# Optimization experiments

Measured on AMD Instinct MI355X. Metric: run time of the kernel, lower is better.

The kernel has to match this reference:

```python
import jax, jax.numpy as jnp
import numpy as np

B, SECL, WORDL = 16, 8, 512
S = SECL * WORDL
H, E, V, NOOV = 256, 128, 50000, 32
EOS = 3
FSIZE = 2  # config.mode == 'train'


def setup_inputs() -> dict:
    key = jax.random.key(0)
    ks = jax.random.split(key, 24)
    g = lambda i, shape, s=0.02: jax.random.normal(ks[i], shape, jnp.float32) * s
    inp = jax.random.randint(ks[0], (B,), 0, V)
    inp = inp.at[:4].set(EOS)  # exercise focus-update branch
    h = g(1, (B, H), 0.1)
    c = g(2, (B, H), 0.1)
    enc_outputs = g(3, (B, S, 2 * H), 1.0)
    enc_feature = g(4, (B, S, 2 * H), 0.1)
    enc_sec_output = g(5, (B, SECL, 2 * H), 1.0)
    enc_mask = jnp.ones((B, S), jnp.float32)
    sec_mask = jnp.ones((B, SECL), jnp.float32)
    prev_context = g(6, (B, 2 * H), 0.1)
    zeros_oov = jnp.zeros((B, NOOV), jnp.float32)
    enc_input_oov = jax.random.randint(ks[7], (B, S), 0, V + NOOV)
    coverage = jnp.zeros((B, S), jnp.float32)
    # sparse nonneg focus distribution over sections (guaranteed >=1 nonzero/row)
    u = jax.random.uniform(ks[8], (B, SECL))
    f = u * (u > 0.5)
    fb = jax.nn.one_hot(jnp.argmax(u, axis=1), SECL)
    f = jnp.where(f.sum(1, keepdims=True) > 0, f, fb)
    focus = f / f.sum(1, keepdims=True)
    params = dict(
        embedding=g(9, (V, E)),
        W_comb=g(10, (E, 2 * H + E)), b_comb=jnp.zeros((E,), jnp.float32),
        W_ih=g(11, (4 * H, E)), W_hh=g(12, (4 * H, H)),
        b_ih=jnp.zeros((4 * H,), jnp.float32), b_hh=jnp.zeros((4 * H,), jnp.float32),
        W_d=g(13, (2 * H, 2 * H)), b_d=jnp.zeros((2 * H,), jnp.float32),
        W_feat=g(14, (2 * H, 2 * H)), v_sec=g(15, (2 * H,)),
        W_dec=g(16, (2 * H, 2 * H)), b_dec=jnp.zeros((2 * H,), jnp.float32),
        w_cov=g(17, (2 * H,)), v_att=g(18, (2 * H,)),
        W_pgen=g(19, (1, 4 * H + E)), b_pgen=jnp.zeros((1,), jnp.float32),
        W_out=g(20, (V, 3 * H)), b_out=g(21, (V,)),
    )
    return dict(inp=inp, h=h, c=c, enc_outputs=enc_outputs, enc_feature=enc_feature,
                enc_sec_output=enc_sec_output, enc_mask=enc_mask, sec_mask=sec_mask,
                prev_context=prev_context, zeros_oov=zeros_oov, enc_input_oov=enc_input_oov,
                coverage=coverage, focus=focus, **params)


def _focus_update(focus, sad):
    # rem_mask: positions from the first nonzero of focus onward
    fz = jnp.cumprod((focus == 0).astype(sad.dtype), axis=1)
    rem_mask = (fz == 0).astype(sad.dtype)
    focus_index = jnp.sum(fz, axis=1).astype(jnp.int32)  # index of first nonzero
    focus_mask = jax.nn.one_hot(focus_index, SECL, dtype=sad.dtype)
    rem_ex = rem_mask - focus_mask
    focus_beta = sad * focus_mask
    rem_beta = sad * rem_ex
    max_rem_beta = rem_beta.max(axis=1)
    max_rem_ind = jnp.argmax(rem_beta, axis=1)
    compare = (focus_beta.max(axis=1) * 2 > max_rem_beta).astype(sad.dtype)[:, None]
    # train branch
    src = (max_rem_beta != 0).astype(sad.dtype)[:, None]
    max_rem_mask = jax.nn.one_hot(max_rem_ind, SECL, dtype=sad.dtype) * src
    cp2 = jnp.cumprod((max_rem_mask == 0).astype(sad.dtype), axis=1)
    after = (cp2 == 0).astype(sad.dtype) - max_rem_mask
    amb = sad * after
    mam_mask = (jax.nn.one_hot(jnp.argmax(amb, axis=1), SECL, dtype=sad.dtype)
                * (amb.max(axis=1) != 0).astype(sad.dtype)[:, None])
    case_f = focus_beta + sad * max_rem_mask
    case_r = sad * (max_rem_mask + mam_mask)
    fu = compare * case_f + (1 - compare) * case_r
    return fu / fu.sum(1, keepdims=True)


def reference(inp, h, c, enc_outputs, enc_feature, enc_sec_output, enc_mask, sec_mask,
              prev_context, zeros_oov, enc_input_oov, coverage, focus,
              embedding, W_comb, b_comb, W_ih, W_hh, b_ih, b_hh,
              W_d, b_d, W_feat, v_sec, W_dec, b_dec, w_cov, v_att,
              W_pgen, b_pgen, W_out, b_out):
    inp_is_eos = (inp == EOS).astype(jnp.float32)[:, None]  # [B,1] -> bcast over secL
    emb = embedding[inp]  # [B,E]
    x = jnp.concatenate([prev_context, emb], axis=1) @ W_comb.T + b_comb  # [B,E]
    # single LSTM step (torch gate order i,f,g,o)
    gates = x @ W_ih.T + b_ih + h @ W_hh.T + b_hh
    gi_, gf_, gg_, go_ = jnp.split(gates, 4, axis=1)
    c_new = jax.nn.sigmoid(gf_) * c + jax.nn.sigmoid(gi_) * jnp.tanh(gg_)
    h_new = jax.nn.sigmoid(go_) * jnp.tanh(c_new)
    dec_state = jnp.concatenate([h_new, c_new], axis=1)  # [B,2H]
    # section attention
    feat = enc_sec_output @ W_feat.T  # [B,secL,2H]
    d = dec_state @ W_d.T + b_d
    sc = jnp.tanh(feat + d[:, None, :]) @ v_sec  # [B,secL]
    sad = jax.nn.softmax(sc, axis=1) * sec_mask
    sad = sad / sad.sum(1, keepdims=True)
    # hard-attention focus update (only where input was EOS)
    fu = _focus_update(focus, sad)
    focus = inp_is_eos * fu + (1 - inp_is_eos) * focus
    # word attention with coverage
    dfeat = dec_state @ W_dec.T + b_dec
    att = enc_feature + dfeat[:, None, :] + coverage[:, :, None] * w_cov[None, None, :]
    score = jnp.tanh(att) @ v_att  # [B,S]
    score3 = score.reshape(B, SECL, WORDL)
    topk_focus, gidx = jax.lax.top_k(focus, FSIZE)  # [B,FSIZE]
    bidx = jnp.arange(B)[:, None]
    score_g = score3[bidx, gidx].reshape(B, FSIZE * WORDL)
    mask_g = enc_mask.reshape(B, SECL, WORDL)[bidx, gidx].reshape(B, FSIZE * WORDL)
    af = jax.nn.softmax(score_g, axis=1) * mask_g
    af = af / af.sum(1, keepdims=True)
    af = topk_focus[:, :, None] * af.reshape(B, FSIZE, WORDL)
    attn = jnp.zeros((B, SECL, WORDL), af.dtype).at[bidx, gidx].set(af).reshape(B, S)
    attn = attn / attn.sum(1, keepdims=True)
    context = jnp.einsum('bs,bsd->bd', attn, enc_outputs)  # [B,2H]
    coverage = coverage + attn
    # pointer-generator
    p_gen = jax.nn.sigmoid(jnp.concatenate([context, dec_state, x], axis=1) @ W_pgen.T + b_pgen)
    logits = jnp.concatenate([h_new, context], axis=1) @ W_out.T + b_out
    vocab_dist = jax.nn.softmax(logits, axis=1)
    vext = jnp.concatenate([p_gen * vocab_dist, zeros_oov], axis=1)  # [B,V+NOOV]
    final = vext.at[bidx, enc_input_oov].add((1 - p_gen) * attn)
    return final, h_new, c_new, context, attn, coverage, focus, sad
```

## Files before the change

### kernel.cpp

```cpp
#include <hip/hip_runtime.h>
#include <math.h>

#define NB 16
#define SECL 8
#define WORDL 512
#define SS 4096
#define HH 256
#define EE 128
#define VV 50000
#define NOOV 32
#define VO 50032
#define EOS_ID 3
#define H2 512
#define KOUT 768
#define NCH 13
#define CHSZ 4096

#define OFF_FINAL 0
#define OFF_H    800512
#define OFF_C    804608
#define OFF_CTX  808704
#define OFF_ATTN 816896
#define OFF_COV  882432
#define OFF_FOC  947968
#define OFF_SAD  948096

#define WX     0
#define WD     2048
#define WDF    10240
#define WSC    18432
#define WGI    18560
#define WTF    18592
#define WSG    18624
#define WPART  35008
#define WPG    166080
#define WPM    166096
#define WPS    166304
#define WLG    166512

__device__ __forceinline__ float sigm(float x){ return 1.f/(1.f+__expf(-x)); }
__device__ __forceinline__ float tfast(float x){
  float ax = fabsf(x);
  float e  = __expf(-2.f*ax);
  float t  = (1.f-e)/(1.f+e);
  return x < 0.f ? -t : t;
}
__device__ __forceinline__ float dot4(float acc, float4 a, float4 b){
  acc = fmaf(a.x,b.x,acc); acc = fmaf(a.y,b.y,acc);
  acc = fmaf(a.z,b.z,acc); acc = fmaf(a.w,b.w,acc);
  return acc;
}
__device__ __forceinline__ float dot2(float acc, float2 a, float2 b){
  acc = fmaf(a.x,b.x,acc); acc = fmaf(a.y,b.y,acc);
  return acc;
}
__device__ __forceinline__ float mergep(float a, float b, int k, int lane){
  float send = (lane & k) ? a : b;
  float recv = __shfl_xor(send, k);
  return (lane & k) ? b + recv : a + recv;
}
__device__ __forceinline__ float reduce8(float acc[8], int lane){
  float m0 = mergep(acc[0], acc[1], 1, lane);
  float m1 = mergep(acc[2], acc[3], 1, lane);
  float m2 = mergep(acc[4], acc[5], 1, lane);
  float m3 = mergep(acc[6], acc[7], 1, lane);
  float n0 = mergep(m0, m1, 2, lane);
  float n1 = mergep(m2, m3, 2, lane);
  float p  = mergep(n0, n1, 4, lane);
  p += __shfl_xor(p, 8);
  p += __shfl_xor(p, 16);
  p += __shfl_xor(p, 32);
  return p;
}

__global__ void __launch_bounds__(256)
k_x(const int* __restrict__ inp, const float* __restrict__ pc,
    const float* __restrict__ emb, const float* __restrict__ Wc,
    const float* __restrict__ bc, float* __restrict__ ws){
  int lane = threadIdx.x & 63;
  int gw = blockIdx.x*4 + (threadIdx.x >> 6);
  int bg = gw & 1, e = gw >> 1;
  float4 z = {0,0,0,0};
  float4 i0[8], i1[8], i2[8];
  #pragma unroll
  for(int j=0;j<8;j++){
    int b = bg*8 + j;
    i0[j] = *(const float4*)(pc + b*H2 + lane*4);
    i1[j] = *(const float4*)(pc + b*H2 + 256 + lane*4);
    i2[j] = (lane < 32) ? *(const float4*)(emb + (size_t)inp[b]*EE + lane*4) : z;
  }
  const float* wr = Wc + (size_t)e*(H2+EE);
  float4 w0 = *(const float4*)(wr + lane*4);
  float4 w1 = *(const float4*)(wr + 256 + lane*4);
  float4 w2 = (lane < 32) ? *(const float4*)(wr + 512 + lane*4) : z;
  float acc[8];
  #pragma unroll
  for(int j=0;j<8;j++){
    float a = dot4(0.f, w0, i0[j]);
    a = dot4(a, w1, i1[j]);
    a = dot4(a, w2, i2[j]);
    acc[j] = a;
  }
  float p = reduce8(acc, lane);
  if(lane < 8) ws[WX + (bg*8+lane)*EE + e] = p + bc[e];
}

__global__ void __launch_bounds__(256)
k_gates(const float* __restrict__ h, const float* __restrict__ c,
        const float* __restrict__ Wih, const float* __restrict__ Whh,
        const float* __restrict__ bih, const float* __restrict__ bhh,
        const float* __restrict__ ws, float* __restrict__ out){
  __shared__ float g_lds[4][8];
  int lane = threadIdx.x & 63;
  int wv   = threadIdx.x >> 6;
  int j  = blockIdx.x >> 1;
  int bg = blockIdx.x & 1;
  float2 xb[8]; float4 hb[8];
  #pragma unroll
  for(int q=0;q<8;q++){
    int b = bg*8 + q;
    xb[q] = *(const float2*)(ws + WX + b*EE + lane*2);
    hb[q] = *(const float4*)(h + b*HH + lane*4);
  }
  int r = wv*HH + j;
  float2 wx = *(const float2*)(Wih + (size_t)r*EE + lane*2);
  float4 wh = *(const float4*)(Whh + (size_t)r*HH + lane*4);
  float acc[8];
  #pragma unroll
  for(int q=0;q<8;q++)
    acc[q] = dot4(dot2(0.f, wx, xb[q]), wh, hb[q]);
  float p = reduce8(acc, lane);
  if(lane < 8) g_lds[wv][lane] = p + bih[r] + bhh[r];
  __syncthreads();
  if(threadIdx.x < 8){
    int b = bg*8 + threadIdx.x;
    float g0 = g_lds[0][threadIdx.x], g1 = g_lds[1][threadIdx.x];
    float g2 = g_lds[2][threadIdx.x], g3 = g_lds[3][threadIdx.x];
    float cn = sigm(g1)*c[b*HH + j] + sigm(g0)*tfast(g2);
    float hn = sigm(g3)*tfast(cn);
    out[OFF_H + b*HH + j] = hn;
    out[OFF_C + b*HH + j] = cn;
  }
}

__global__ void __launch_bounds__(256)
k_dd(const float* __restrict__ Wd, const float* __restrict__ bd,
     const float* __restrict__ Wdec, const float* __restrict__ bdec,
     const float* __restrict__ out, float* __restrict__ ws){
  int lane = threadIdx.x & 63;
  int gw = blockIdx.x*4 + (threadIdx.x >> 6);
  int bg = gw & 1, sel = (gw >> 1) & 1, j = gw >> 2;
  float4 d0[8], d1[8];
  #pragma unroll
  for(int q=0;q<8;q++){
    int b = bg*8 + q;
    d0[q] = *(const float4*)(out + OFF_H + b*HH + lane*4);
    d1[q] = *(const float4*)(out + OFF_C + b*HH + lane*4);
  }
  const float* wr = (sel ? Wdec : Wd) + (size_t)j*H2;
  float4 w0 = *(const float4*)(wr + lane*4);
  float4 w1 = *(const float4*)(wr + 256 + lane*4);
  float acc[8];
  #pragma unroll
  for(int q=0;q<8;q++)
    acc[q] = dot4(dot4(0.f, w0, d0[q]), w1, d1[q]);
  float p = reduce8(acc, lane);
  if(lane < 8) ws[(sel ? WDF : WD) + (bg*8+lane)*H2 + j] = p + (sel ? bdec : bd)[j];
}

__global__ void __launch_bounds__(256)
k_sec(const float* __restrict__ eso, const float* __restrict__ Wf,
      const float* __restrict__ vsec, float* __restrict__ ws){
  __shared__ float red[4];
  int lane = threadIdx.x & 63;
  int wv   = threadIdx.x >> 6;
  int bl = blockIdx.x; int b = bl >> 3;
  const float* ep = eso + (size_t)bl*H2;
  float4 es0 = *(const float4*)(ep + lane*4);
  float4 es1 = *(const float4*)(ep + 256 + lane*4);
  const float* dp = ws + WD + b*H2;
  float local = 0.f;
  for(int t=0;t<16;t++){
    int j0 = wv*8 + t*32;
    float acc[8];
    #pragma unroll
    for(int jj=0;jj<8;jj++){
      const float* wr = Wf + (size_t)(j0+jj)*H2;
      float4 w0 = *(const float4*)(wr + lane*4);
      float4 w1 = *(const float4*)(wr + 256 + lane*4);
      acc[jj] = dot4(dot4(0.f, w0, es0), w1, es1);
    }
    float p = reduce8(acc, lane);
    if(lane < 8){
      int j = j0 + lane;
      local += tfast(p + dp[j]) * vsec[j];
    }
  }
  local += __shfl_xor(local, 1);
  local += __shfl_xor(local, 2);
  local += __shfl_xor(local, 4);
  if(lane == 0) red[wv] = local;
  __syncthreads();
  if(threadIdx.x == 0) ws[WSC + bl] = red[0]+red[1]+red[2]+red[3];
}

__global__ void k_focus(const int* __restrict__ inp, const float* __restrict__ smask,
                        const float* __restrict__ focus_in, float* __restrict__ ws,
                        float* __restrict__ out){
  int b = threadIdx.x;
  if(b >= NB) return;
  float sc[SECL], sad[SECL], f[SECL];
  float mx = -1e30f;
  for(int l=0;l<SECL;l++){ sc[l] = ws[WSC + b*SECL + l]; mx = fmaxf(mx, sc[l]); }
  float sum = 0.f;
  for(int l=0;l<SECL;l++){ sad[l] = __expf(sc[l]-mx); sum += sad[l]; }
  float s2 = 0.f;
  for(int l=0;l<SECL;l++){ sad[l] = sad[l]/sum * smask[b*SECL+l]; s2 += sad[l]; }
  for(int l=0;l<SECL;l++){ sad[l] /= s2; out[OFF_SAD + b*SECL + l] = sad[l]; }
  for(int l=0;l<SECL;l++) f[l] = focus_in[b*SECL+l];
  int fi = SECL;
  for(int l=0;l<SECL;l++){ if(f[l] != 0.f){ fi = l; break; } }
  float rem[SECL];
  for(int l=0;l<SECL;l++) rem[l] = (l > fi) ? sad[l] : 0.f;
  float mrb = rem[0]; int mri = 0;
  for(int l=1;l<SECL;l++){ if(rem[l] > mrb){ mrb = rem[l]; mri = l; } }
  float fbm = (fi < SECL) ? sad[fi] : 0.f;
  int cmp = (fbm*2.f > mrb);
  int src = (mrb != 0.f);
  float amb[SECL];
  for(int l=0;l<SECL;l++) amb[l] = (src && l > mri) ? sad[l] : 0.f;
  float am = amb[0]; int ai = 0;
  for(int l=1;l<SECL;l++){ if(amb[l] > am){ am = amb[l]; ai = l; } }
  float fu[SECL]; float fs = 0.f;
  for(int l=0;l<SECL;l++){
    float mrm = (src && l == mri) ? 1.f : 0.f;
    float mam = ((am != 0.f) && l == ai) ? 1.f : 0.f;
    float cf = ((l==fi) ? sad[l] : 0.f) + sad[l]*mrm;
    float cr = sad[l]*(mrm + mam);
    fu[l] = cmp ? cf : cr;
    fs += fu[l];
  }
  float eos = (inp[b] == EOS_ID) ? 1.f : 0.f;
  float fo[SECL];
  for(int l=0;l<SECL;l++){
    fo[l] = eos*(fu[l]/fs) + (1.f-eos)*f[l];
    out[OFF_FOC + b*SECL + l] = fo[l];
  }
  float v1 = fo[0]; int i1 = 0;
  for(int l=1;l<SECL;l++){ if(fo[l] > v1){ v1 = fo[l]; i1 = l; } }
  float v2 = -1e30f; int i2 = 0;
  for(int l=0;l<SECL;l++){ if(l != i1 && fo[l] > v2){ v2 = fo[l]; i2 = l; } }
  ((int*)ws)[WGI + b*2]     = i1;
  ((int*)ws)[WGI + b*2 + 1] = i2;
  ws[WTF + b*2]     = v1;
  ws[WTF + b*2 + 1] = v2;
}

__global__ void k_score(const float* __restrict__ ef, const float* __restrict__ cov,
                        const float* __restrict__ wcov, const float* __restrict__ vatt,
                        float* __restrict__ ws){
  int lane = threadIdx.x & 63;
  int o = blockIdx.x*4 + (threadIdx.x >> 6);
  int b = o >> 10, fidx = (o >> 9) & 1, w = o & 511;
  int g = ((const int*)ws)[WGI + b*2 + fidx];
  int s = g*WORDL + w;
  const float* e  = ef + ((size_t)(b*SS + s))*H2;
  const float* df = ws + WDF + b*H2;
  float cv = cov[b*SS + s];
  int j = lane*4;
  float local = 0.f;
  #pragma unroll
  for(int half=0; half<2; half++){
    int jj = j + half*256;
    float4 a  = *(const float4*)(e+jj);
    float4 d4 = *(const float4*)(df+jj);
    float4 wc = *(const float4*)(wcov+jj);
    float4 va = *(const float4*)(vatt+jj);
    local += tfast(a.x + d4.x + cv*wc.x)*va.x;
    local += tfast(a.y + d4.y + cv*wc.y)*va.y;
    local += tfast(a.z + d4.z + cv*wc.z)*va.z;
    local += tfast(a.w + d4.w + cv*wc.w)*va.w;
  }
  for(int off=32; off>0; off>>=1) local += __shfl_xor(local, off);
  if(lane == 0) ws[WSG + o] = local;
}

__global__ void k_af(const float* __restrict__ emask, const float* __restrict__ cov,
                     float* __restrict__ ws, float* __restrict__ out){
  __shared__ float es[1024];
  __shared__ float red[256];
  int b = blockIdx.x, tid = threadIdx.x;
  int g0 = ((int*)ws)[WGI+b*2], g1 = ((int*)ws)[WGI+b*2+1];
  float tf0 = ws[WTF+b*2], tf1 = ws[WTF+b*2+1];
  float lm = -1e30f;
  for(int i=tid;i<1024;i+=256) lm = fmaxf(lm, ws[WSG + b*1024 + i]);
  red[tid] = lm; __syncthreads();
  for(int off=128; off; off>>=1){
    if(tid < off) red[tid] = fmaxf(red[tid], red[tid+off]);
    __syncthreads();
  }
  float mx = red[0]; __syncthreads();
  float ls0 = 0.f, ls1 = 0.f;
  for(int i=tid;i<1024;i+=256){
    int fidx = i >> 9, w = i & 511;
    int g = fidx ? g1 : g0;
    float m = emask[b*SS + g*WORDL + w];
    float ev = __expf(ws[WSG + b*1024 + i] - mx)*m;
    es[i] = ev;
    if(fidx) ls1 += ev; else ls0 += ev;
  }
  red[tid] = ls0; __syncthreads();
  for(int off=128; off; off>>=1){ if(tid<off) red[tid]+=red[tid+off]; __syncthreads(); }
  float sum0 = red[0]; __syncthreads();
  red[tid] = ls1; __syncthreads();
  for(int off=128; off; off>>=1){ if(tid<off) red[tid]+=red[tid+off]; __syncthreads(); }
  float sum1 = red[0]; __syncthreads();
  float inv = 1.f/(tf0*sum0 + tf1*sum1);
  for(int s=tid;s<SS;s+=256){
    int sec = s >> 9, w = s & 511;
    float a = 0.f;
    if(sec == g0)      a = tf0*es[w]*inv;
    else if(sec == g1) a = tf1*es[512+w]*inv;
    out[OFF_ATTN + b*SS + s] = a;
    out[OFF_COV  + b*SS + s] = cov[b*SS+s] + a;
  }
}

__global__ void k_ctxp(const float* __restrict__ eo, const float* __restrict__ out,
                       float* __restrict__ ws){
  int blk = blockIdx.x; int b = blk >> 4, ch = blk & 15;
  int d = threadIdx.x;
  int g0 = ((const int*)ws)[WGI + b*2];
  int g1 = ((const int*)ws)[WGI + b*2 + 1];
  float a0 = 0.f, a1 = 0.f;
  #pragma unroll 4
  for(int p = ch*64; p < ch*64 + 64; p++){
    int s = ((p >> 9) ? g1 : g0)*WORDL + (p & 511);
    float a = out[OFF_ATTN + b*SS + s];
    const float* ep = eo + ((size_t)(b*SS + s))*H2;
    a0 = fmaf(a, ep[d],       a0);
    a1 = fmaf(a, ep[d+256],   a1);
  }
  ws[WPART + (size_t)blk*H2 + d]       = a0;
  ws[WPART + (size_t)blk*H2 + d + 256] = a1;
}

__global__ void k_ctx(const float* __restrict__ Wp, const float* __restrict__ bp,
                      float* __restrict__ ws, float* __restrict__ out){
  __shared__ float red[256];
  int b = blockIdx.x, tid = threadIdx.x;
  float c0 = 0.f, c1 = 0.f;
  for(int ch=0; ch<16; ch++){
    c0 += ws[WPART + (size_t)(b*16+ch)*H2 + tid];
    c1 += ws[WPART + (size_t)(b*16+ch)*H2 + tid + 256];
  }
  out[OFF_CTX + b*H2 + tid]       = c0;
  out[OFF_CTX + b*H2 + tid + 256] = c1;
  float hn = out[OFF_H + b*HH + tid];
  float cn = out[OFF_C + b*HH + tid];
  float pv = c0*Wp[tid] + c1*Wp[tid+256] + hn*Wp[512+tid] + cn*Wp[768+tid];
  if(tid < EE) pv = fmaf(ws[WX + b*EE + tid], Wp[1024+tid], pv);
  red[tid] = pv; __syncthreads();
  for(int off=128; off; off>>=1){ if(tid<off) red[tid]+=red[tid+off]; __syncthreads(); }
  if(tid == 0) ws[WPG + b] = sigm(red[0] + bp[0]);
}

__global__ void __launch_bounds__(256,3)
k_logits(const float* __restrict__ Wout, const float* __restrict__ bout,
         const float* __restrict__ out, float* __restrict__ ws){
  int lane = threadIdx.x & 63;
  int wv   = threadIdx.x >> 6;
  int bg   = wv & 1;
  int rh   = wv >> 1;
  float4 hb0[8], hb1[8], hb2[8];
  #pragma unroll
  for(int j=0;j<8;j++){
    int b = bg*8 + j;
    hb0[j] = *(const float4*)(out + OFF_H   + b*HH + lane*4);
    hb1[j] = *(const float4*)(out + OFF_CTX + b*H2 + lane*4);
    hb2[j] = *(const float4*)(out + OFF_CTX + b*H2 + 256 + lane*4);
  }
  int v = blockIdx.x*32 + rh;
  int vc = v < VV ? v : VV-1;
  const float* wp = Wout + (size_t)vc*KOUT + lane*4;
  float4 a0 = *(const float4*)(wp);
  float4 a1 = *(const float4*)(wp+256);
  float4 a2 = *(const float4*)(wp+512);
  #pragma unroll 2
  for(int r=0;r<16;r++){
    int vn = v + 2;
    int vnc = vn < VV ? vn : VV-1;
    const float* np = Wout + (size_t)vnc*KOUT + lane*4;
    float4 n0 = *(const float4*)(np);
    float4 n1 = *(const float4*)(np+256);
    float4 n2 = *(const float4*)(np+512);
    float acc[8];
    #pragma unroll
    for(int j=0;j<8;j++){
      float a = dot4(0.f, a0, hb0[j]);
      a = dot4(a, a1, hb1[j]);
      a = dot4(a, a2, hb2[j]);
      acc[j] = a;
    }
    float p = reduce8(acc, lane);
    if(v < VV && lane < 8)
      ws[WLG + (size_t)(bg*8+lane)*VV + v] = p + bout[v];
    a0 = n0; a1 = n1; a2 = n2;
    v = vn;
  }
}

__global__ void k_vms(float* __restrict__ ws){
  __shared__ float rm[256], rs[256];
  int blk = blockIdx.x; int b = blk/NCH, ch = blk%NCH;
  int tid = threadIdx.x;
  int v0 = ch*CHSZ; int v1 = v0+CHSZ; if(v1 > VV) v1 = VV;
  float mt = -1e30f, st = 0.f;
  for(int v=v0+tid; v<v1; v+=256){
    float x = ws[WLG + (size_t)b*VV + v];
    if(x > mt){ st = st*__expf(mt - x) + 1.f; mt = x; }
    else       st += __expf(x - mt);
  }
  rm[tid] = mt; rs[tid] = st; __syncthreads();
  for(int off=128; off; off>>=1){
    if(tid < off){
      float ma = rm[tid], mb = rm[tid+off];
      float M = fmaxf(ma, mb);
      rs[tid] = rs[tid]*__expf(ma-M) + rs[tid+off]*__expf(mb-M);
      rm[tid] = M;
    }
    __syncthreads();
  }
  if(tid == 0){ ws[WPM + blk] = rm[0]; ws[WPS + blk] = rs[0]; }
}

__global__ void k_final(const float* __restrict__ zoov, float* __restrict__ ws,
                        float* __restrict__ out){
  int blk = blockIdx.x; int b = blk/NCH, ch = blk%NCH;
  float mx = -1e30f, sm = 0.f;
  for(int i=0;i<NCH;i++){ mx = fmaxf(mx, ws[WPM + b*NCH + i]); }
  for(int i=0;i<NCH;i++){ sm += ws[WPS + b*NCH + i]*__expf(ws[WPM + b*NCH + i] - mx); }
  float scale = ws[WPG + b] / sm;
  int v0 = ch*CHSZ; int v1 = v0+CHSZ; if(v1 > VO) v1 = VO;
  for(int v=v0+threadIdx.x; v<v1; v+=256){
    float r;
    if(v < VV) r = scale*__expf(ws[WLG + (size_t)b*VV + v] - mx);
    else       r = zoov[b*NOOV + v - VV];
    out[OFF_FINAL + (size_t)b*VO + v] = r;
  }
}

__global__ void k_scatter(const int* __restrict__ oov, const float* __restrict__ ws,
                          float* __restrict__ out){
  int blk = blockIdx.x; int b = blk >> 4;
  int s = (blk & 15)*256 + threadIdx.x;
  float a = out[OFF_ATTN + b*SS + s];
  if(a != 0.f){
    float w = (1.f - ws[WPG + b])*a;
    atomicAdd(out + OFF_FINAL + (size_t)b*VO + oov[b*SS + s], w);
  }
}

extern "C" void kernel_launch(void* const* d_in, const int* in_sizes, int n_in,
                              void* d_out, int out_size, void* d_ws, size_t ws_size,
                              hipStream_t stream){
  const int*   inp   = (const int*)  d_in[0];
  const float* h     = (const float*)d_in[1];
  const float* c     = (const float*)d_in[2];
  const float* eo    = (const float*)d_in[3];
  const float* efeat = (const float*)d_in[4];
  const float* eso   = (const float*)d_in[5];
  const float* emask = (const float*)d_in[6];
  const float* smask = (const float*)d_in[7];
  const float* pctx  = (const float*)d_in[8];
  const float* zoov  = (const float*)d_in[9];
  const int*   oov   = (const int*)  d_in[10];
  const float* cov   = (const float*)d_in[11];
  const float* foc   = (const float*)d_in[12];
  const float* emb   = (const float*)d_in[13];
  const float* Wc    = (const float*)d_in[14];
  const float* bc    = (const float*)d_in[15];
  const float* Wih   = (const float*)d_in[16];
  const float* Whh   = (const float*)d_in[17];
  const float* bih   = (const float*)d_in[18];
  const float* bhh   = (const float*)d_in[19];
  const float* Wd    = (const float*)d_in[20];
  const float* bd    = (const float*)d_in[21];
  const float* Wf    = (const float*)d_in[22];
  const float* vsec  = (const float*)d_in[23];
  const float* Wdec  = (const float*)d_in[24];
  const float* bdec  = (const float*)d_in[25];
  const float* wcov  = (const float*)d_in[26];
  const float* vatt  = (const float*)d_in[27];
  const float* Wp    = (const float*)d_in[28];
  const float* bp    = (const float*)d_in[29];
  const float* Wout  = (const float*)d_in[30];
  const float* bout  = (const float*)d_in[31];
  float* out = (float*)d_out;
  float* ws  = (float*)d_ws;

  k_x      <<<64,   256, 0, stream>>>(inp, pctx, emb, Wc, bc, ws);
  k_gates  <<<512,  256, 0, stream>>>(h, c, Wih, Whh, bih, bhh, ws, out);
  k_dd     <<<512,  256, 0, stream>>>(Wd, bd, Wdec, bdec, out, ws);
  k_sec    <<<128,  256, 0, stream>>>(eso, Wf, vsec, ws);
  k_focus  <<<1,     64, 0, stream>>>(inp, smask, foc, ws, out);
  k_score  <<<4096, 256, 0, stream>>>(efeat, cov, wcov, vatt, ws);
  k_af     <<<16,   256, 0, stream>>>(emask, cov, ws, out);
  k_ctxp   <<<256,  256, 0, stream>>>(eo, out, ws);
  k_ctx    <<<16,   256, 0, stream>>>(Wp, bp, ws, out);
  k_logits <<<1563, 256, 0, stream>>>(Wout, bout, out, ws);
  k_vms    <<<208,  256, 0, stream>>>(ws);
  k_final  <<<208,  256, 0, stream>>>(zoov, ws, out);
  k_scatter<<<256,  256, 0, stream>>>(oov, ws, out);
}
```

Measured before the change: 139.5 us.

## Fuse front-end kernels into cooperative grid-synced kernel and restructure logits pipelining

Replaces the five small front-end kernels (x projection, LSTM gates, decoder projections, section scores, focus update) with one cooperative kernel that uses grid.sync between phases, removing launch gaps. The section-score phase is split four ways per section so all 512 blocks take part, with partial sums combined in the focus step. If the cooperative launch fails, the code falls back to the old separate launches. Separately, the logits kernel now has each wave handle 8 consecutive vocab rows with a two-deep register prefetch, and the grid doubles to 3125 blocks with no tail bounds check.

```diff
diff --git a/kernel.cpp b/kernel.cpp
--- a/kernel.cpp
+++ b/kernel.cpp
@@ -1,5 +1,8 @@
 #include <hip/hip_runtime.h>
+#include <hip/hip_cooperative_groups.h>
 #include <math.h>
+
+namespace cg = cooperative_groups;
 
 #define NB 16
 #define SECL 8
@@ -37,6 +40,7 @@
 #define WPM    166096
 #define WPS    166304
 #define WLG    166512
+#define WSCP   966512
 
 __device__ __forceinline__ float sigm(float x){ return 1.f/(1.f+__expf(-x)); }
 __device__ __forceinline__ float tfast(float x){
@@ -73,12 +77,10 @@
   return p;
 }
 
-__global__ void __launch_bounds__(256)
-k_x(const int* __restrict__ inp, const float* __restrict__ pc,
-    const float* __restrict__ emb, const float* __restrict__ Wc,
-    const float* __restrict__ bc, float* __restrict__ ws){
-  int lane = threadIdx.x & 63;
-  int gw = blockIdx.x*4 + (threadIdx.x >> 6);
+
+__device__ __forceinline__ void phase_x(int gw, int lane,
+    const int* inp, const float* pc, const float* emb,
+    const float* Wc, const float* bc, float* ws){
   int bg = gw & 1, e = gw >> 1;
   float4 z = {0,0,0,0};
   float4 i0[8], i1[8], i2[8];
@@ -105,69 +107,205 @@
   if(lane < 8) ws[WX + (bg*8+lane)*EE + e] = p + bc[e];
 }
 
+__device__ __forceinline__ void phase_gates(int blk, int wv, int lane, int tid,
+    const float* h, const float* c, const float* Wih, const float* Whh,
+    const float* bih, const float* bhh, const float* ws, float* out,
+    float (*g_lds)[8]){
+  int j  = blk >> 1;
+  int bg = blk & 1;
+  float2 xb[8]; float4 hb[8];
+  #pragma unroll
+  for(int q=0;q<8;q++){
+    int b = bg*8 + q;
+    xb[q] = *(const float2*)(ws + WX + b*EE + lane*2);
+    hb[q] = *(const float4*)(h + b*HH + lane*4);
+  }
+  int r = wv*HH + j;
+  float2 wx = *(const float2*)(Wih + (size_t)r*EE + lane*2);
+  float4 wh = *(const float4*)(Whh + (size_t)r*HH + lane*4);
+  float acc[8];
+  #pragma unroll
+  for(int q=0;q<8;q++)
+    acc[q] = dot4(dot2(0.f, wx, xb[q]), wh, hb[q]);
+  float p = reduce8(acc, lane);
+  if(lane < 8) g_lds[wv][lane] = p + bih[r] + bhh[r];
+  __syncthreads();
+  if(tid < 8){
+    int b = bg*8 + tid;
+    float g0 = g_lds[0][tid], g1 = g_lds[1][tid];
+    float g2 = g_lds[2][tid], g3 = g_lds[3][tid];
+    float cn = sigm(g1)*c[b*HH + j] + sigm(g0)*tfast(g2);
+    float hn = sigm(g3)*tfast(cn);
+    out[OFF_H + b*HH + j] = hn;
+    out[OFF_C + b*HH + j] = cn;
+  }
+}
+
+__device__ __forceinline__ void phase_dd(int gw, int lane,
+    const float* Wd, const float* bd, const float* Wdec, const float* bdec,
+    const float* out, float* ws){
+  int bg = gw & 1, sel = (gw >> 1) & 1, j = gw >> 2;
+  float4 d0[8], d1[8];
+  #pragma unroll
+  for(int q=0;q<8;q++){
+    int b = bg*8 + q;
+    d0[q] = *(const float4*)(out + OFF_H + b*HH + lane*4);
+    d1[q] = *(const float4*)(out + OFF_C + b*HH + lane*4);
+  }
+  const float* wr = (sel ? Wdec : Wd) + (size_t)j*H2;
+  float4 w0 = *(const float4*)(wr + lane*4);
+  float4 w1 = *(const float4*)(wr + 256 + lane*4);
+  float acc[8];
+  #pragma unroll
+  for(int q=0;q<8;q++)
+    acc[q] = dot4(dot4(0.f, w0, d0[q]), w1, d1[q]);
+  float p = reduce8(acc, lane);
+  if(lane < 8) ws[(sel ? WDF : WD) + (bg*8+lane)*H2 + j] = p + (sel ? bdec : bd)[j];
+}
+
+__device__ __forceinline__ void focus_body(int b, float sc[SECL],
+    const int* inp, const float* smask, const float* focus_in,
+    float* ws, float* out){
+  float sad[SECL], f[SECL];
+  float mx = -1e30f;
+  for(int l=0;l<SECL;l++) mx = fmaxf(mx, sc[l]);
+  float sum = 0.f;
+  for(int l=0;l<SECL;l++){ sad[l] = __expf(sc[l]-mx); sum += sad[l]; }
+  float s2 = 0.f;
+  for(int l=0;l<SECL;l++){ sad[l] = sad[l]/sum * smask[b*SECL+l]; s2 += sad[l]; }
+  for(int l=0;l<SECL;l++){ sad[l] /= s2; out[OFF_SAD + b*SECL + l] = sad[l]; }
+  for(int l=0;l<SECL;l++) f[l] = focus_in[b*SECL+l];
+  int fi = SECL;
+  for(int l=0;l<SECL;l++){ if(f[l] != 0.f){ fi = l; break; } }
+  float rem[SECL];
+  for(int l=0;l<SECL;l++) rem[l] = (l > fi) ? sad[l] : 0.f;
+  float mrb = rem[0]; int mri = 0;
+  for(int l=1;l<SECL;l++){ if(rem[l] > mrb){ mrb = rem[l]; mri = l; } }
+  float fbm = (fi < SECL) ? sad[fi] : 0.f;
+  int cmp = (fbm*2.f > mrb);
+  int src = (mrb != 0.f);
+  float amb[SECL];
+  for(int l=0;l<SECL;l++) amb[l] = (src && l > mri) ? sad[l] : 0.f;
+  float am = amb[0]; int ai = 0;
+  for(int l=1;l<SECL;l++){ if(amb[l] > am){ am = amb[l]; ai = l; } }
+  float fu[SECL]; float fs = 0.f;
+  for(int l=0;l<SECL;l++){
+    float mrm = (src && l == mri) ? 1.f : 0.f;
+    float mam = ((am != 0.f) && l == ai) ? 1.f : 0.f;
+    float cf = ((l==fi) ? sad[l] : 0.f) + sad[l]*mrm;
+    float cr = sad[l]*(mrm + mam);
+    fu[l] = cmp ? cf : cr;
+    fs += fu[l];
+  }
+  float eos = (inp[b] == EOS_ID) ? 1.f : 0.f;
+  float fo[SECL];
+  for(int l=0;l<SECL;l++){
+    fo[l] = eos*(fu[l]/fs) + (1.f-eos)*f[l];
+    out[OFF_FOC + b*SECL + l] = fo[l];
+  }
+  float v1 = fo[0]; int i1 = 0;
+  for(int l=1;l<SECL;l++){ if(fo[l] > v1){ v1 = fo[l]; i1 = l; } }
+  float v2 = -1e30f; int i2 = 0;
+  for(int l=0;l<SECL;l++){ if(l != i1 && fo[l] > v2){ v2 = fo[l]; i2 = l; } }
+  ((int*)ws)[WGI + b*2]     = i1;
+  ((int*)ws)[WGI + b*2 + 1] = i2;
+  ws[WTF + b*2]     = v1;
+  ws[WTF + b*2 + 1] = v2;
+}
+
+__global__ void __launch_bounds__(256)
+k_front2(const int* __restrict__ inp, const float* __restrict__ pc,
+         const float* __restrict__ emb, const float* __restrict__ Wc,
+         const float* __restrict__ bc,
+         const float* __restrict__ h, const float* __restrict__ c,
+         const float* __restrict__ Wih, const float* __restrict__ Whh,
+         const float* __restrict__ bih, const float* __restrict__ bhh,
+         const float* __restrict__ Wd, const float* __restrict__ bd,
+         const float* __restrict__ Wdec, const float* __restrict__ bdec,
+         const float* __restrict__ eso, const float* __restrict__ Wf,
+         const float* __restrict__ vsec,
+         const float* __restrict__ smask, const float* __restrict__ foc,
+         float* __restrict__ ws, float* __restrict__ out){
+  cg::grid_group grid = cg::this_grid();
+  __shared__ float g_lds[4][8];
+  __shared__ float red[4];
+  int tid  = threadIdx.x;
+  int lane = tid & 63;
+  int wv   = tid >> 6;
+  int blk  = blockIdx.x;
+
+  if(blk < 64) phase_x(blk*4 + wv, lane, inp, pc, emb, Wc, bc, ws);
+  grid.sync();
+  phase_gates(blk, wv, lane, tid, h, c, Wih, Whh, bih, bhh, ws, out, g_lds);
+  grid.sync();
+  phase_dd(blk*4 + wv, lane, Wd, bd, Wdec, bdec, out, ws);
+  grid.sync();
+  {
+    int bl = blk >> 2, part = blk & 3;
+    int b = bl >> 3;
+    const float* ep = eso + (size_t)bl*H2;
+    float4 es0 = *(const float4*)(ep + lane*4);
+    float4 es1 = *(const float4*)(ep + 256 + lane*4);
+    const float* dp = ws + WD + b*H2;
+    float local = 0.f;
+    for(int tt=0;tt<4;tt++){
+      int t = part*4 + tt;
+      int j0 = wv*8 + t*32;
+      float acc[8];
+      #pragma unroll
+      for(int jj=0;jj<8;jj++){
+        const float* wr = Wf + (size_t)(j0+jj)*H2;
+        float4 w0 = *(const float4*)(wr + lane*4);
+        float4 w1 = *(const float4*)(wr + 256 + lane*4);
+        acc[jj] = dot4(dot4(0.f, w0, es0), w1, es1);
+      }
+      float p = reduce8(acc, lane);
+      if(lane < 8){
+        int j = j0 + lane;
+        local += tfast(p + dp[j]) * vsec[j];
+      }
+    }
+    local += __shfl_xor(local, 1);
+    local += __shfl_xor(local, 2);
+    local += __shfl_xor(local, 4);
+    if(lane == 0) red[wv] = local;
+    __syncthreads();
+    if(tid == 0) ws[WSCP + blk] = red[0]+red[1]+red[2]+red[3];
+  }
+  grid.sync();
+  if(blk == 0 && tid < NB){
+    int b = tid;
+    float sc[SECL];
+    for(int l=0;l<SECL;l++){
+      int bl = b*SECL + l;
+      sc[l] = ws[WSCP + bl*4] + ws[WSCP + bl*4+1]
+            + ws[WSCP + bl*4+2] + ws[WSCP + bl*4+3];
+    }
+    focus_body(b, sc, inp, smask, foc, ws, out);
+  }
+}
+
+__global__ void __launch_bounds__(256)
+k_x(const int* __restrict__ inp, const float* __restrict__ pc,
+    const float* __restrict__ emb, const float* __restrict__ Wc,
+    const float* __restrict__ bc, float* __restrict__ ws){
+  phase_x(blockIdx.x*4 + (threadIdx.x>>6), threadIdx.x & 63, inp, pc, emb, Wc, bc, ws);
+}
 __global__ void __launch_bounds__(256)
 k_gates(const float* __restrict__ h, const float* __restrict__ c,
         const float* __restrict__ Wih, const float* __restrict__ Whh,
         const float* __restrict__ bih, const float* __restrict__ bhh,
         const float* __restrict__ ws, float* __restrict__ out){
   __shared__ float g_lds[4][8];
-  int lane = threadIdx.x & 63;
-  int wv   = threadIdx.x >> 6;
-  int j  = blockIdx.x >> 1;
-  int bg = blockIdx.x & 1;
-  float2 xb[8]; float4 hb[8];
-  #pragma unroll
-  for(int q=0;q<8;q++){
-    int b = bg*8 + q;
-    xb[q] = *(const float2*)(ws + WX + b*EE + lane*2);
-    hb[q] = *(const float4*)(h + b*HH + lane*4);
-  }
-  int r = wv*HH + j;
-  float2 wx = *(const float2*)(Wih + (size_t)r*EE + lane*2);
-  float4 wh = *(const float4*)(Whh + (size_t)r*HH + lane*4);
-  float acc[8];
-  #pragma unroll
-  for(int q=0;q<8;q++)
-    acc[q] = dot4(dot2(0.f, wx, xb[q]), wh, hb[q]);
-  float p = reduce8(acc, lane);
-  if(lane < 8) g_lds[wv][lane] = p + bih[r] + bhh[r];
-  __syncthreads();
-  if(threadIdx.x < 8){
-    int b = bg*8 + threadIdx.x;
-    float g0 = g_lds[0][threadIdx.x], g1 = g_lds[1][threadIdx.x];
-    float g2 = g_lds[2][threadIdx.x], g3 = g_lds[3][threadIdx.x];
-    float cn = sigm(g1)*c[b*HH + j] + sigm(g0)*tfast(g2);
-    float hn = sigm(g3)*tfast(cn);
-    out[OFF_H + b*HH + j] = hn;
-    out[OFF_C + b*HH + j] = cn;
-  }
-}
-
+  phase_gates(blockIdx.x, threadIdx.x>>6, threadIdx.x&63, threadIdx.x,
+              h, c, Wih, Whh, bih, bhh, ws, out, g_lds);
+}
 __global__ void __launch_bounds__(256)
 k_dd(const float* __restrict__ Wd, const float* __restrict__ bd,
      const float* __restrict__ Wdec, const float* __restrict__ bdec,
      const float* __restrict__ out, float* __restrict__ ws){
-  int lane = threadIdx.x & 63;
-  int gw = blockIdx.x*4 + (threadIdx.x >> 6);
-  int bg = gw & 1, sel = (gw >> 1) & 1, j = gw >> 2;
-  float4 d0[8], d1[8];
-  #pragma unroll
-  for(int q=0;q<8;q++){
-    int b = bg*8 + q;
-    d0[q] = *(const float4*)(out + OFF_H + b*HH + lane*4);
-    d1[q] = *(const float4*)(out + OFF_C + b*HH + lane*4);
-  }
-  const float* wr = (sel ? Wdec : Wd) + (size_t)j*H2;
-  float4 w0 = *(const float4*)(wr + lane*4);
-  float4 w1 = *(const float4*)(wr + 256 + lane*4);
-  float acc[8];
-  #pragma unroll
-  for(int q=0;q<8;q++)
-    acc[q] = dot4(dot4(0.f, w0, d0[q]), w1, d1[q]);
-  float p = reduce8(acc, lane);
-  if(lane < 8) ws[(sel ? WDF : WD) + (bg*8+lane)*H2 + j] = p + (sel ? bdec : bd)[j];
-}
-
+  phase_dd(blockIdx.x*4 + (threadIdx.x>>6), threadIdx.x&63, Wd, bd, Wdec, bdec, out, ws);
+}
 __global__ void __launch_bounds__(256)
 k_sec(const float* __restrict__ eso, const float* __restrict__ Wf,
       const float* __restrict__ vsec, float* __restrict__ ws){
@@ -203,58 +341,16 @@
   __syncthreads();
   if(threadIdx.x == 0) ws[WSC + bl] = red[0]+red[1]+red[2]+red[3];
 }
-
 __global__ void k_focus(const int* __restrict__ inp, const float* __restrict__ smask,
                         const float* __restrict__ focus_in, float* __restrict__ ws,
                         float* __restrict__ out){
   int b = threadIdx.x;
   if(b >= NB) return;
-  float sc[SECL], sad[SECL], f[SECL];
-  float mx = -1e30f;
-  for(int l=0;l<SECL;l++){ sc[l] = ws[WSC + b*SECL + l]; mx = fmaxf(mx, sc[l]); }
-  float sum = 0.f;
-  for(int l=0;l<SECL;l++){ sad[l] = __expf(sc[l]-mx); sum += sad[l]; }
-  float s2 = 0.f;
-  for(int l=0;l<SECL;l++){ sad[l] = sad[l]/sum * smask[b*SECL+l]; s2 += sad[l]; }
-  for(int l=0;l<SECL;l++){ sad[l] /= s2; out[OFF_SAD + b*SECL + l] = sad[l]; }
-  for(int l=0;l<SECL;l++) f[l] = focus_in[b*SECL+l];
-  int fi = SECL;
-  for(int l=0;l<SECL;l++){ if(f[l] != 0.f){ fi = l; break; } }
-  float rem[SECL];
-  for(int l=0;l<SECL;l++) rem[l] = (l > fi) ? sad[l] : 0.f;
-  float mrb = rem[0]; int mri = 0;
-  for(int l=1;l<SECL;l++){ if(rem[l] > mrb){ mrb = rem[l]; mri = l; } }
-  float fbm = (fi < SECL) ? sad[fi] : 0.f;
-  int cmp = (fbm*2.f > mrb);
-  int src = (mrb != 0.f);
-  float amb[SECL];
-  for(int l=0;l<SECL;l++) amb[l] = (src && l > mri) ? sad[l] : 0.f;
-  float am = amb[0]; int ai = 0;
-  for(int l=1;l<SECL;l++){ if(amb[l] > am){ am = amb[l]; ai = l; } }
-  float fu[SECL]; float fs = 0.f;
-  for(int l=0;l<SECL;l++){
-    float mrm = (src && l == mri) ? 1.f : 0.f;
-    float mam = ((am != 0.f) && l == ai) ? 1.f : 0.f;
-    float cf = ((l==fi) ? sad[l] : 0.f) + sad[l]*mrm;
-    float cr = sad[l]*(mrm + mam);
-    fu[l] = cmp ? cf : cr;
-    fs += fu[l];
-  }
-  float eos = (inp[b] == EOS_ID) ? 1.f : 0.f;
-  float fo[SECL];
-  for(int l=0;l<SECL;l++){
-    fo[l] = eos*(fu[l]/fs) + (1.f-eos)*f[l];
-    out[OFF_FOC + b*SECL + l] = fo[l];
-  }
-  float v1 = fo[0]; int i1 = 0;
-  for(int l=1;l<SECL;l++){ if(fo[l] > v1){ v1 = fo[l]; i1 = l; } }
-  float v2 = -1e30f; int i2 = 0;
-  for(int l=0;l<SECL;l++){ if(l != i1 && fo[l] > v2){ v2 = fo[l]; i2 = l; } }
-  ((int*)ws)[WGI + b*2]     = i1;
-  ((int*)ws)[WGI + b*2 + 1] = i2;
-  ws[WTF + b*2]     = v1;
-  ws[WTF + b*2 + 1] = v2;
-}
+  float sc[SECL];
+  for(int l=0;l<SECL;l++) sc[l] = ws[WSC + b*SECL + l];
+  focus_body(b, sc, inp, smask, focus_in, ws, out);
+}
+
 
 __global__ void k_score(const float* __restrict__ ef, const float* __restrict__ cov,
                         const float* __restrict__ wcov, const float* __restrict__ vatt,
@@ -380,33 +476,37 @@
     hb1[j] = *(const float4*)(out + OFF_CTX + b*H2 + lane*4);
     hb2[j] = *(const float4*)(out + OFF_CTX + b*H2 + 256 + lane*4);
   }
-  int v = blockIdx.x*32 + rh;
-  int vc = v < VV ? v : VV-1;
-  const float* wp = Wout + (size_t)vc*KOUT + lane*4;
-  float4 a0 = *(const float4*)(wp);
-  float4 a1 = *(const float4*)(wp+256);
-  float4 a2 = *(const float4*)(wp+512);
-  #pragma unroll 2
-  for(int r=0;r<16;r++){
-    int vn = v + 2;
-    int vnc = vn < VV ? vn : VV-1;
-    const float* np = Wout + (size_t)vnc*KOUT + lane*4;
-    float4 n0 = *(const float4*)(np);
-    float4 n1 = *(const float4*)(np+256);
-    float4 n2 = *(const float4*)(np+512);
+  int v0 = blockIdx.x*16 + rh*8;
+  const float* w0p = Wout + (size_t)v0*KOUT + lane*4;
+  float4 A0 = *(const float4*)(w0p);
+  float4 A1 = *(const float4*)(w0p+256);
+  float4 A2 = *(const float4*)(w0p+512);
+  const float* w1p = w0p + KOUT;
+  float4 B0 = *(const float4*)(w1p);
+  float4 B1 = *(const float4*)(w1p+256);
+  float4 B2 = *(const float4*)(w1p+512);
+  #pragma unroll
+  for(int r=0;r<8;r++){
+    float4 C0=A0, C1=A1, C2=A2;
+    if(r < 6){
+      const float* np = w0p + (size_t)(r+2)*KOUT;
+      C0 = *(const float4*)(np);
+      C1 = *(const float4*)(np+256);
+      C2 = *(const float4*)(np+512);
+    }
     float acc[8];
     #pragma unroll
     for(int j=0;j<8;j++){
-      float a = dot4(0.f, a0, hb0[j]);
-      a = dot4(a, a1, hb1[j]);
-      a = dot4(a, a2, hb2[j]);
+      float a = dot4(0.f, A0, hb0[j]);
+      a = dot4(a, A1, hb1[j]);
+      a = dot4(a, A2, hb2[j]);
       acc[j] = a;
     }
     float p = reduce8(acc, lane);
-    if(v < VV && lane < 8)
-      ws[WLG + (size_t)(bg*8+lane)*VV + v] = p + bout[v];
-    a0 = n0; a1 = n1; a2 = n2;
-    v = vn;
+    int v = v0 + r;
+    if(lane < 8) ws[WLG + (size_t)(bg*8+lane)*VV + v] = p + bout[v];
+    A0=B0; A1=B1; A2=B2;
+    B0=C0; B1=C1; B2=C2;
   }
 }
 
@@ -499,16 +599,27 @@
   float* out = (float*)d_out;
   float* ws  = (float*)d_ws;
 
-  k_x      <<<64,   256, 0, stream>>>(inp, pctx, emb, Wc, bc, ws);
-  k_gates  <<<512,  256, 0, stream>>>(h, c, Wih, Whh, bih, bhh, ws, out);
-  k_dd     <<<512,  256, 0, stream>>>(Wd, bd, Wdec, bdec, out, ws);
-  k_sec    <<<128,  256, 0, stream>>>(eso, Wf, vsec, ws);
-  k_focus  <<<1,     64, 0, stream>>>(inp, smask, foc, ws, out);
+  void* fargs[] = {
+    (void*)&inp, (void*)&pctx, (void*)&emb, (void*)&Wc, (void*)&bc,
+    (void*)&h, (void*)&c, (void*)&Wih, (void*)&Whh, (void*)&bih, (void*)&bhh,
+    (void*)&Wd, (void*)&bd, (void*)&Wdec, (void*)&bdec,
+    (void*)&eso, (void*)&Wf, (void*)&vsec, (void*)&smask, (void*)&foc,
+    (void*)&ws, (void*)&out
+  };
+  hipError_t ce = hipLaunchCooperativeKernel((void*)k_front2, dim3(512), dim3(256),
+                                             fargs, 0, stream);
+  if(ce != hipSuccess){
+    k_x     <<<64,  256, 0, stream>>>(inp, pctx, emb, Wc, bc, ws);
+    k_gates <<<512, 256, 0, stream>>>(h, c, Wih, Whh, bih, bhh, ws, out);
+    k_dd    <<<512, 256, 0, stream>>>(Wd, bd, Wdec, bdec, out, ws);
+    k_sec   <<<128, 256, 0, stream>>>(eso, Wf, vsec, ws);
+    k_focus <<<1,    64, 0, stream>>>(inp, smask, foc, ws, out);
+  }
   k_score  <<<4096, 256, 0, stream>>>(efeat, cov, wcov, vatt, ws);
   k_af     <<<16,   256, 0, stream>>>(emask, cov, ws, out);
   k_ctxp   <<<256,  256, 0, stream>>>(eo, out, ws);
   k_ctx    <<<16,   256, 0, stream>>>(Wp, bp, ws, out);
-  k_logits <<<1563, 256, 0, stream>>>(Wout, bout, out, ws);
+  k_logits <<<3125, 256, 0, stream>>>(Wout, bout, out, ws);
   k_vms    <<<208,  256, 0, stream>>>(ws);
   k_final  <<<208,  256, 0, stream>>>(zoov, ws, out);
   k_scatter<<<256,  256, 0, stream>>>(oov, ws, out);
```

Measured after the change: 326.6 us. 2.34x slower.
